# Optimization experiments

Measured on AMD Instinct MI355X. Metric: run time of the kernel, lower is better.

Reference implementation:

```python
import jax, jax.numpy as jnp
import numpy as np

EMBED = 192
D_INNER = 2 * EMBED          # expand=2
D_STATE = 4                  # low_rank
D_CONV = 4
DT_RANK = (EMBED + 15) // 16 # ceil(192/16) = 12
N_MIX = 2
RANK = 4                     # LowRankProjection rank
B_, H_, W_ = 8, 64, 64


def setup_inputs() -> dict:
    key = jax.random.key(0)
    ks = jax.random.split(key, 16)
    s = lambda *sh: 1.0 / np.sqrt(sh[-1])
    inp = {
        "x": jax.random.normal(ks[0], (B_, EMBED, H_, W_), jnp.float32),
        # stacked per-mixer Mamba params (leading dim N_MIX)
        "in_proj_w": jax.random.normal(ks[1], (N_MIX, 2 * D_INNER, EMBED), jnp.float32) * s(EMBED),
        "conv_w": jax.random.normal(ks[2], (N_MIX, D_INNER, D_CONV), jnp.float32) * s(D_CONV),
        "conv_b": jnp.zeros((N_MIX, D_INNER), jnp.float32),
        "x_proj_w": jax.random.normal(ks[3], (N_MIX, DT_RANK + 2 * D_STATE, D_INNER), jnp.float32) * s(D_INNER),
        "dt_proj_w": jax.random.normal(ks[4], (N_MIX, D_INNER, DT_RANK), jnp.float32) * s(DT_RANK),
        "dt_proj_b": jax.random.uniform(ks[5], (N_MIX, D_INNER), jnp.float32, -4.0, -2.0),
        "A_log": jnp.tile(jnp.log(jnp.arange(1, D_STATE + 1, dtype=jnp.float32))[None, None, :], (N_MIX, D_INNER, 1)),
        "D": jnp.ones((N_MIX, D_INNER), jnp.float32),
        "out_proj_w": jax.random.normal(ks[6], (N_MIX, EMBED, D_INNER), jnp.float32) * s(D_INNER),
        # LowRankProjection
        "U_w": jax.random.normal(ks[7], (RANK, EMBED), jnp.float32) * s(EMBED),
        "V_w": jax.random.normal(ks[8], (EMBED, RANK), jnp.float32) * s(RANK),
        # LayerNorm
        "ln_g": jnp.ones((EMBED,), jnp.float32),
        "ln_b": jnp.zeros((EMBED,), jnp.float32),
    }
    return inp


def _silu(x):
    return x * jax.nn.sigmoid(x)


def _mamba(x, in_proj_w, conv_w, conv_b, x_proj_w, dt_proj_w, dt_proj_b, A_log, D, out_proj_w):
    # x: (B, L, d_model)
    B, L, _ = x.shape
    xz = jnp.einsum("bld,ed->ble", x, in_proj_w)          # (B, L, 2*d_inner)
    xin, z = jnp.split(xz, 2, axis=-1)
    # causal depthwise conv over L
    xt = jnp.transpose(xin, (0, 2, 1))                      # (B, d_inner, L)
    xc = jax.lax.conv_general_dilated(
        xt, conv_w[:, None, :], window_strides=(1,), padding=[(D_CONV - 1, 0)],
        feature_group_count=D_INNER, dimension_numbers=("NCH", "OIH", "NCH"))
    xa = _silu(jnp.transpose(xc + conv_b[None, :, None], (0, 2, 1)))  # (B, L, d_inner)
    x_dbl = jnp.einsum("bld,ed->ble", xa, x_proj_w)         # (B, L, dt_rank+2*d_state)
    dt_lr = x_dbl[..., :DT_RANK]
    Bm = x_dbl[..., DT_RANK:DT_RANK + D_STATE]              # (B, L, d_state)
    Cm = x_dbl[..., DT_RANK + D_STATE:]                     # (B, L, d_state)
    dt = jax.nn.softplus(jnp.einsum("blr,dr->bld", dt_lr, dt_proj_w) + dt_proj_b)  # (B, L, d_inner)
    A = -jnp.exp(A_log)                                     # (d_inner, d_state)
    dA = jnp.exp(dt[..., None] * A)                         # (B, L, d_inner, d_state)
    dBu = dt[..., None] * Bm[:, :, None, :] * xa[..., None]  # (B, L, d_inner, d_state)

    def step(h, inputs):
        dA_i, dBu_i, C_i = inputs                           # (B,d_inner,d_state),(B,d_inner,d_state),(B,d_state)
        h = dA_i * h + dBu_i
        y = jnp.einsum("bds,bs->bd", h, C_i)
        return h, y

    h0 = jnp.zeros((B, D_INNER, D_STATE), x.dtype)
    _, ys = jax.lax.scan(step, h0, (jnp.moveaxis(dA, 1, 0), jnp.moveaxis(dBu, 1, 0), jnp.moveaxis(Cm, 1, 0)))
    y = jnp.moveaxis(ys, 0, 1) + xa * D                     # (B, L, d_inner)
    y = y * _silu(z)
    return jnp.einsum("ble,de->bld", y, out_proj_w)         # (B, L, d_model)


def reference(x, in_proj_w, conv_w, conv_b, x_proj_w, dt_proj_w, dt_proj_b,
              A_log, D, out_proj_w, U_w, V_w, ln_g, ln_b):
    residual = x
    B, C, H, W = x.shape
    h = jnp.transpose(x, (0, 2, 3, 1)).reshape(B, H * W, C)
    for i in range(N_MIX):
        h = _mamba(h, in_proj_w[i], conv_w[i], conv_b[i], x_proj_w[i], dt_proj_w[i],
                   dt_proj_b[i], A_log[i], D[i], out_proj_w[i])
    # low-rank projection
    h = jnp.einsum("blr,dr->bld", jnp.einsum("blc,rc->blr", h, U_w), V_w)
    h = jnp.transpose(h.reshape(B, H, W, C), (0, 3, 1, 2)) + residual
    # LayerNorm over channels
    hc = jnp.transpose(h, (0, 2, 3, 1))
    mu = hc.mean(-1, keepdims=True)
    var = ((hc - mu) ** 2).mean(-1, keepdims=True)
    hc = (hc - mu) * jax.lax.rsqrt(var + 1e-5) * ln_g + ln_b
    return jnp.transpose(hc, (0, 3, 1, 2))
```

## Files before the change

kernel.cpp:

```cpp
#include <hip/hip_runtime.h>
#include <hip/hip_bf16.h>
#include <cstdint>

#define EMBED   192
#define DINNER  384
#define DSTATE  4
#define DCONV   4
#define DTRANK  12
#define NMIX    2
#define RANK    4
#define BB      8
#define LL      4096
#define NBL     (BB*LL)
#define NCHUNK  128
#define CLEN    32
#define RSTR    36

typedef __attribute__((ext_vector_type(8))) short short8;
typedef __attribute__((ext_vector_type(4))) float float4v;

static __device__ __forceinline__ ushort f2b(float f) {
    __hip_bfloat16 h = __float2bfloat16(f);
    return *(ushort*)&h;
}
static __device__ __forceinline__ float b2f(ushort u) {
    __hip_bfloat16 h;
    *(ushort*)&h = u;
    return __bfloat162float(h);
}
static __device__ __forceinline__ float bs2f(short s) {
    ushort u = (ushort)s;
    return b2f(u);
}

#define PREP_N0 294912
#define PREP_N1 147456
#define PREP_N2 24576
#define PREP_N3 24576
#define PREP_N4 3072
__global__ __launch_bounds__(256) void k_prep(const float* __restrict__ in_proj_w,
                                              const float* __restrict__ out_proj_w,
                                              const float* __restrict__ x_proj_w,
                                              const float* __restrict__ dt_proj_w,
                                              const float* __restrict__ conv_w,
                                              ushort* __restrict__ wi,
                                              ushort* __restrict__ wo,
                                              ushort* __restrict__ xpwb,
                                              ushort* __restrict__ dtwpad,
                                              float* __restrict__ cwt) {
    int i = blockIdx.x * 256 + threadIdx.x;
    if (i < PREP_N0) {
        wi[i] = f2b(in_proj_w[i]);
        return;
    }
    i -= PREP_N0;
    if (i < PREP_N1) {
        wo[i] = f2b(out_proj_w[i]);
        return;
    }
    i -= PREP_N1;
    if (i < PREP_N2) {
        int mix = i / (32 * 384);
        int rem = i % (32 * 384);
        int e = rem / 384, k = rem % 384;
        xpwb[i] = (e < 20) ? f2b(x_proj_w[(size_t)mix * 20 * 384 + e * 384 + k]) : (ushort)0;
        return;
    }
    i -= PREP_N2;
    if (i < PREP_N3) {
        int mix = i / (384 * 32);
        int rem = i % (384 * 32);
        int n = rem / 32, r = rem % 32;
        dtwpad[i] = (r < DTRANK) ? f2b(dt_proj_w[(size_t)mix * 384 * DTRANK + n * DTRANK + r])
                                 : (ushort)0;
        return;
    }
    i -= PREP_N3;
    if (i < PREP_N4) {
        int mix = i / (DCONV * DINNER);
        int rem = i % (DCONV * DINNER);
        int k = rem / DINNER, d = rem % DINNER;
        cwt[i] = conv_w[(size_t)mix * DINNER * DCONV + d * DCONV + k];
    }
}

__global__ __launch_bounds__(256) void k_transpose(const float* __restrict__ x,
                                                   ushort* __restrict__ h0b) {
    __shared__ float tile[32][33];
    int b  = blockIdx.z;
    int c0 = blockIdx.y * 32;
    int l0 = blockIdx.x * 32;
    int tx = threadIdx.x;
    int ty = threadIdx.y;
    #pragma unroll
    for (int i = 0; i < 4; i++) {
        int c = c0 + ty + i * 8;
        tile[ty + i * 8][tx] = x[((size_t)b * EMBED + c) * LL + l0 + tx];
    }
    __syncthreads();
    #pragma unroll
    for (int i = 0; i < 4; i++) {
        int l = l0 + ty + i * 8;
        h0b[((size_t)b * LL + l) * EMBED + c0 + tx] = f2b(tile[tx][ty + i * 8]);
    }
}

template<int TN, int WRN>
__global__ __launch_bounds__(256) void k_gemm_bf16(const ushort* __restrict__ A, int lda,
                                                   const ushort* __restrict__ Bw, int ldb,
                                                   float* __restrict__ C, int ldc,
                                                   ushort* __restrict__ Cb, int ldcb,
                                                   int K) {
    constexpr int WRM = 4 / WRN;
    constexpr int WM  = 128 / WRM;
    constexpr int MT  = WM / 16;
    __shared__ ushort As[128][40];
    __shared__ ushort Bs[TN][40];
    int tid  = threadIdx.x;
    int lane = tid & 63;
    int wave = tid >> 6;
    int wmo = (wave / WRN) * WM;
    int wno = (wave % WRN) * 64;
    int m0 = blockIdx.y * 128;
    int n0 = blockIdx.x * TN;

    float4v acc[MT][4];
    #pragma unroll
    for (int i = 0; i < MT; i++)
        #pragma unroll
        for (int j = 0; j < 4; j++)
            acc[i][j] = (float4v){0.f, 0.f, 0.f, 0.f};

    for (int k0 = 0; k0 < K; k0 += 32) {
        #pragma unroll
        for (int i = 0; i < 2; i++) {
            int idx = tid + i * 256;
            int r = idx >> 2, sg = idx & 3;
            *(short8*)&As[r][sg * 8] =
                *(const short8*)(A + (size_t)(m0 + r) * lda + k0 + sg * 8);
        }
        #pragma unroll
        for (int i = 0; i < TN / 64; i++) {
            int idx = tid + i * 256;
            int r = idx >> 2, sg = idx & 3;
            *(short8*)&Bs[r][sg * 8] =
                *(const short8*)(Bw + (size_t)(n0 + r) * ldb + k0 + sg * 8);
        }
        __syncthreads();
        short8 av[MT], bv[4];
        #pragma unroll
        for (int i = 0; i < MT; i++)
            av[i] = *(const short8*)&As[wmo + i * 16 + (lane & 15)][(lane >> 4) * 8];
        #pragma unroll
        for (int j = 0; j < 4; j++)
            bv[j] = *(const short8*)&Bs[wno + j * 16 + (lane & 15)][(lane >> 4) * 8];
        #pragma unroll
        for (int i = 0; i < MT; i++)
            #pragma unroll
            for (int j = 0; j < 4; j++)
                acc[i][j] = __builtin_amdgcn_mfma_f32_16x16x32_bf16(
                    av[i], bv[j], acc[i][j], 0, 0, 0);
        __syncthreads();
    }

    #pragma unroll
    for (int i = 0; i < MT; i++) {
        int rbase = m0 + wmo + i * 16 + (lane >> 4) * 4;
        #pragma unroll
        for (int j = 0; j < 4; j++) {
            int col = n0 + wno + j * 16 + (lane & 15);
            #pragma unroll
            for (int r = 0; r < 4; r++) {
                float v = acc[i][j][r];
                if (C)  C[(size_t)(rbase + r) * ldc + col] = v;
                if (Cb) Cb[(size_t)(rbase + r) * ldcb + col] = f2b(v);
            }
        }
    }
}

__global__ __launch_bounds__(256) void k_conv_silu(const ushort* __restrict__ xz,
                                                   const float* __restrict__ cwt,
                                                   const float* __restrict__ cb,
                                                   ushort* __restrict__ xa) {
    int t   = blockIdx.x * 256 + threadIdx.x;
    int g   = t % 48;
    int blc = t / 48;
    int d0  = g * 8;
    int lc  = blc % (LL / 8);
    int b   = blc / (LL / 8);
    int l0  = lc * 8;

    float wk[4][8], bias[8];
    #pragma unroll
    for (int k = 0; k < 4; k++) {
        float4v wa = *(const float4v*)(cwt + k * DINNER + d0);
        float4v wb = *(const float4v*)(cwt + k * DINNER + d0 + 4);
        #pragma unroll
        for (int j = 0; j < 4; j++) { wk[k][j] = wa[j]; wk[k][j + 4] = wb[j]; }
    }
    {
        float4v ba = *(const float4v*)(cb + d0);
        float4v bb = *(const float4v*)(cb + d0 + 4);
        #pragma unroll
        for (int j = 0; j < 4; j++) { bias[j] = ba[j]; bias[j + 4] = bb[j]; }
    }

    float r0[8] = {}, r1[8] = {}, r2[8] = {};
    const ushort* px = xz + ((size_t)(b * LL + l0)) * 768 + d0;
    if (l0 > 0) {
        short8 v;
        v = *(const short8*)(px - 3 * 768);
        #pragma unroll
        for (int j = 0; j < 8; j++) r0[j] = bs2f(v[j]);
        v = *(const short8*)(px - 2 * 768);
        #pragma unroll
        for (int j = 0; j < 8; j++) r1[j] = bs2f(v[j]);
        v = *(const short8*)(px - 1 * 768);
        #pragma unroll
        for (int j = 0; j < 8; j++) r2[j] = bs2f(v[j]);
    }
    ushort* po = xa + ((size_t)(b * LL + l0)) * DINNER + d0;
    #pragma unroll
    for (int i = 0; i < 8; i++) {
        short8 v = *(const short8*)(px + (size_t)i * 768);
        float cur[8];
        #pragma unroll
        for (int j = 0; j < 8; j++) cur[j] = bs2f(v[j]);
        short8 ov;
        #pragma unroll
        for (int j = 0; j < 8; j++) {
            float a = bias[j] + wk[0][j] * r0[j] + wk[1][j] * r1[j]
                    + wk[2][j] * r2[j] + wk[3][j] * cur[j];
            float sv = a / (1.f + __expf(-a));
            ov[j] = (short)f2b(sv);
        }
        *(short8*)(po + (size_t)i * DINNER) = ov;
        #pragma unroll
        for (int j = 0; j < 8; j++) { r0[j] = r1[j]; r1[j] = r2[j]; r2[j] = cur[j]; }
    }
}

__global__ __launch_bounds__(256) void k_xproj_mfma(const ushort* __restrict__ xa,
                                                    const ushort* __restrict__ xpwb,
                                                    float* __restrict__ xdb32) {
    __shared__ ushort As[128][40];
    __shared__ ushort Bs[32][40];
    int tid  = threadIdx.x;
    int lane = tid & 63;
    int wave = tid >> 6;
    int m0 = blockIdx.x * 128;
    float4v acc[2][2];
    #pragma unroll
    for (int i = 0; i < 2; i++)
        #pragma unroll
        for (int j = 0; j < 2; j++)
            acc[i][j] = (float4v){0.f, 0.f, 0.f, 0.f};
    for (int k0 = 0; k0 < 384; k0 += 32) {
        #pragma unroll
        for (int i = 0; i < 2; i++) {
            int idx = tid + i * 256;
            int r = idx >> 2, sg = idx & 3;
            *(short8*)&As[r][sg * 8] =
                *(const short8*)(xa + (size_t)(m0 + r) * 384 + k0 + sg * 8);
        }
        if (tid < 128) {
            int r = tid >> 2, sg = tid & 3;
            *(short8*)&Bs[r][sg * 8] =
                *(const short8*)(xpwb + (size_t)r * 384 + k0 + sg * 8);
        }
        __syncthreads();
        short8 av[2], bv[2];
        #pragma unroll
        for (int i = 0; i < 2; i++)
            av[i] = *(const short8*)&As[wave * 32 + i * 16 + (lane & 15)][(lane >> 4) * 8];
        #pragma unroll
        for (int j = 0; j < 2; j++)
            bv[j] = *(const short8*)&Bs[j * 16 + (lane & 15)][(lane >> 4) * 8];
        #pragma unroll
        for (int i = 0; i < 2; i++)
            #pragma unroll
            for (int j = 0; j < 2; j++)
                acc[i][j] = __builtin_amdgcn_mfma_f32_16x16x32_bf16(
                    av[i], bv[j], acc[i][j], 0, 0, 0);
        __syncthreads();
    }
    #pragma unroll
    for (int i = 0; i < 2; i++) {
        int rbase = m0 + wave * 32 + i * 16 + (lane >> 4) * 4;
        #pragma unroll
        for (int j = 0; j < 2; j++) {
            int col = j * 16 + (lane & 15);
            #pragma unroll
            for (int r = 0; r < 4; r++)
                xdb32[(size_t)(rbase + r) * 32 + col] = acc[i][j][r];
        }
    }
}

static __device__ __forceinline__ void dt_mfma_tile(const float* __restrict__ rows,
                                                    const ushort* __restrict__ dtwpad,
                                                    const float* __restrict__ dtb,
                                                    ushort* __restrict__ dtS,
                                                    int wave, int lane) {
    int mcol = lane & 15;
    int quad = lane >> 4;
    #pragma unroll
    for (int nt = 0; nt < 4; nt++) {
        int n = wave * 64 + nt * 16 + mcol;
        short8 bv = *(const short8*)(dtwpad + (size_t)n * 32 + quad * 8);
        float bias = dtb[n];
        #pragma unroll
        for (int mt = 0; mt < 2; mt++) {
            float4v a0 = *(const float4v*)&rows[(mt * 16 + mcol) * RSTR + quad * 8];
            float4v a1 = *(const float4v*)&rows[(mt * 16 + mcol) * RSTR + quad * 8 + 4];
            short8 av;
            #pragma unroll
            for (int j = 0; j < 4; j++) {
                av[j]     = (short)f2b(a0[j]);
                av[j + 4] = (short)f2b(a1[j]);
            }
            float4v acc = (float4v){0.f, 0.f, 0.f, 0.f};
            acc = __builtin_amdgcn_mfma_f32_16x16x32_bf16(av, bv, acc, 0, 0, 0);
            #pragma unroll
            for (int r = 0; r < 4; r++) {
                float s = acc[r] + bias;
                float sp = fmaxf(s, 0.f) + __logf(1.f + __expf(-fabsf(s)));
                dtS[(mt * 16 + quad * 4 + r) * DINNER + n] = f2b(sp);
            }
        }
    }
}

static __device__ __forceinline__ bool as_is_harmonic(const float* As) {
    return fabsf(As[1] - 2.f * As[0]) <= 1e-5f * fabsf(As[1]) + 1e-12f
        && fabsf(As[2] - 3.f * As[0]) <= 1e-5f * fabsf(As[2]) + 1e-12f
        && fabsf(As[3] - 4.f * As[0]) <= 1e-5f * fabsf(As[3]) + 1e-12f;
}

__global__ __launch_bounds__(384) void k_scan_local(const ushort* __restrict__ xa,
                                                    const float* __restrict__ xdb32,
                                                    const ushort* __restrict__ dtwpad,
                                                    const float* __restrict__ dtb,
                                                    const float* __restrict__ A_log,
                                                    float* __restrict__ carryT,
                                                    float* __restrict__ carryH) {
    int d     = threadIdx.x;
    int lane  = d & 63;
    int wave  = d >> 6;
    int chunk = blockIdx.x;
    int b     = blockIdx.y;
    __shared__ float rows[CLEN * RSTR];
    __shared__ ushort dtS[CLEN * DINNER];
    size_t rbase = ((size_t)b * LL + (size_t)chunk * CLEN) * 32;
    for (int i = d; i < CLEN * 32; i += 384) {
        int l = i >> 5, e = i & 31;
        rows[l * RSTR + e] = xdb32[rbase + i];
    }
    float As[DSTATE];
    #pragma unroll
    for (int s = 0; s < DSTATE; s++) As[s] = -__expf(A_log[d * DSTATE + s]);
    bool fastA = as_is_harmonic(As);
    __syncthreads();
    dt_mfma_tile(rows, dtwpad, dtb, dtS, wave, lane);
    __syncthreads();
    float h[DSTATE] = {0.f, 0.f, 0.f, 0.f};
    float T = 0.f;
    size_t mbase = (size_t)b * LL + (size_t)chunk * CLEN;
    for (int l = 0; l < CLEN; l++) {
        float dtvv = b2f(dtS[l * DINNER + d]);
        float xav  = b2f(xa[(mbase + l) * DINNER + d]);
        float du   = dtvv * xav;
        T += dtvv;
        const float* row = &rows[l * RSTR];
        float da[DSTATE];
        if (fastA) {
            float p = __expf(dtvv * As[0]);
            da[0] = p; da[1] = p * p; da[2] = da[1] * p; da[3] = da[2] * p;
        } else {
            #pragma unroll
            for (int s = 0; s < DSTATE; s++) da[s] = __expf(dtvv * As[s]);
        }
        #pragma unroll
        for (int s = 0; s < DSTATE; s++)
            h[s] = da[s] * h[s] + du * row[DTRANK + s];
    }
    size_t cb = ((size_t)chunk * BB + b);
    carryT[cb * 384 + d] = T;
    float4v hv = {h[0], h[1], h[2], h[3]};
    *(float4v*)(carryH + cb * 1536 + d * 4) = hv;
}

__global__ __launch_bounds__(256) void k_scan_combine(const float* __restrict__ carryT,
                                                      const float* __restrict__ carryH,
                                                      const float* __restrict__ A_log,
                                                      float* __restrict__ carryI) {
    int c   = blockIdx.x * 256 + threadIdx.x;
    int b   = c / 1536;
    int rem = c - b * 1536;
    int d   = rem >> 2;
    float As = -__expf(A_log[rem]);
    float hrun = 0.f;
    for (int k = 0; k < NCHUNK; k++) {
        size_t o = (size_t)k * BB + b;
        float T  = carryT[o * 384 + d];
        float Hk = carryH[o * 1536 + rem];
        carryI[o * 1536 + rem] = hrun;
        hrun = __expf(As * T) * hrun + Hk;
    }
}

__global__ __launch_bounds__(384) void k_scan_final(const ushort* __restrict__ xa,
                                                    const ushort* __restrict__ xz,
                                                    const float* __restrict__ xdb32,
                                                    const ushort* __restrict__ dtwpad,
                                                    const float* __restrict__ dtb,
                                                    const float* __restrict__ A_log,
                                                    const float* __restrict__ Dp,
                                                    const float* __restrict__ carryI,
                                                    ushort* __restrict__ y) {
    int d     = threadIdx.x;
    int lane  = d & 63;
    int wave  = d >> 6;
    int chunk = blockIdx.x;
    int b     = blockIdx.y;
    __shared__ float rows[CLEN * RSTR];
    __shared__ ushort dtS[CLEN * DINNER];
    size_t rbase = ((size_t)b * LL + (size_t)chunk * CLEN) * 32;
    for (int i = d; i < CLEN * 32; i += 384) {
        int l = i >> 5, e = i & 31;
        rows[l * RSTR + e] = xdb32[rbase + i];
    }
    float As[DSTATE];
    #pragma unroll
    for (int s = 0; s < DSTATE; s++) As[s] = -__expf(A_log[d * DSTATE + s]);
    bool fastA = as_is_harmonic(As);
    float Dd = Dp[d];
    float4v hv = *(const float4v*)(carryI + ((size_t)chunk * BB + b) * 1536 + d * 4);
    float h[DSTATE];
    #pragma unroll
    for (int s = 0; s < DSTATE; s++) h[s] = hv[s];
    __syncthreads();
    dt_mfma_tile(rows, dtwpad, dtb, dtS, wave, lane);
    __syncthreads();
    size_t mbase = (size_t)b * LL + (size_t)chunk * CLEN;
    for (int l = 0; l < CLEN; l++) {
        size_t m = mbase + l;
        float dtvv = b2f(dtS[l * DINNER + d]);
        float xav  = b2f(xa[m * DINNER + d]);
        float du   = dtvv * xav;
        const float* row = &rows[l * RSTR];
        float da[DSTATE];
        if (fastA) {
            float p = __expf(dtvv * As[0]);
            da[0] = p; da[1] = p * p; da[2] = da[1] * p; da[3] = da[2] * p;
        } else {
            #pragma unroll
            for (int s = 0; s < DSTATE; s++) da[s] = __expf(dtvv * As[s]);
        }
        float yv = 0.f;
        #pragma unroll
        for (int s = 0; s < DSTATE; s++) {
            h[s] = da[s] * h[s] + du * row[DTRANK + s];
            yv  += h[s] * row[DTRANK + DSTATE + s];
        }
        yv += xav * Dd;
        float zv = b2f(xz[m * 768 + DINNER + d]);
        yv *= zv / (1.f + __expf(-zv));
        y[m * DINNER + d] = f2b(yv);
    }
}

__global__ __launch_bounds__(256) void k_tail(const ushort* __restrict__ h1b,
                                              const ushort* __restrict__ h0b,
                                              const float* __restrict__ U,
                                              const float* __restrict__ V,
                                              const float* __restrict__ g,
                                              const float* __restrict__ be,
                                              float* __restrict__ out) {
    __shared__ float tile[EMBED * 65];
    int tid  = threadIdx.x;
    int lane = tid & 63;
    int wave = tid >> 6;
    int b  = blockIdx.y;
    int l0 = blockIdx.x * 64;
    for (int t = 0; t < 16; t++) {
        int lloc = wave * 16 + t;
        size_t m = (size_t)b * LL + l0 + lloc;
        float hv[3];
        #pragma unroll
        for (int i = 0; i < 3; i++) hv[i] = b2f(h1b[m * EMBED + lane + 64 * i]);
        float r[RANK];
        #pragma unroll
        for (int j = 0; j < RANK; j++) {
            float p = 0.f;
            #pragma unroll
            for (int i = 0; i < 3; i++) p += hv[i] * U[j * EMBED + lane + 64 * i];
            #pragma unroll
            for (int off = 1; off < 64; off <<= 1) p += __shfl_xor(p, off);
            r[j] = p;
        }
        float u[3], s1 = 0.f, s2 = 0.f;
        #pragma unroll
        for (int i = 0; i < 3; i++) {
            int c = lane + 64 * i;
            float v = r[0] * V[c * 4 + 0] + r[1] * V[c * 4 + 1]
                    + r[2] * V[c * 4 + 2] + r[3] * V[c * 4 + 3];
            u[i] = v + b2f(h0b[m * EMBED + c]);
            s1 += u[i];
            s2 += u[i] * u[i];
        }
        #pragma unroll
        for (int off = 1; off < 64; off <<= 1) {
            s1 += __shfl_xor(s1, off);
            s2 += __shfl_xor(s2, off);
        }
        float mean = s1 * (1.f / EMBED);
        float var  = s2 * (1.f / EMBED) - mean * mean;
        float inv  = rsqrtf(var + 1e-5f);
        #pragma unroll
        for (int i = 0; i < 3; i++) {
            int c = lane + 64 * i;
            tile[c * 65 + lloc] = (u[i] - mean) * inv * g[c] + be[c];
        }
    }
    __syncthreads();
    for (int i = tid; i < EMBED * 64; i += 256) {
        int c = i >> 6, l = i & 63;
        out[((size_t)(b * EMBED + c)) * LL + l0 + l] = tile[c * 65 + l];
    }
}

extern "C" void kernel_launch(void* const* d_in, const int* in_sizes, int n_in,
                              void* d_out, int out_size, void* d_ws, size_t ws_size,
                              hipStream_t stream) {
    const float* x          = (const float*)d_in[0];
    const float* in_proj_w  = (const float*)d_in[1];
    const float* conv_w     = (const float*)d_in[2];
    const float* conv_b     = (const float*)d_in[3];
    const float* x_proj_w   = (const float*)d_in[4];
    const float* dt_proj_w  = (const float*)d_in[5];
    const float* dt_proj_b  = (const float*)d_in[6];
    const float* A_log      = (const float*)d_in[7];
    const float* Dp         = (const float*)d_in[8];
    const float* out_proj_w = (const float*)d_in[9];
    const float* U_w        = (const float*)d_in[10];
    const float* V_w        = (const float*)d_in[11];
    const float* ln_g       = (const float*)d_in[12];
    const float* ln_b       = (const float*)d_in[13];
    float* out = (float*)d_out;

    float* ws    = (float*)d_ws;
    float* xdb32 = ws;
    float* carryT = xdb32 + (size_t)NBL * 32;
    float* carryH = carryT + (size_t)NCHUNK * BB * DINNER;
    float* carryI = carryH + (size_t)NCHUNK * BB * DINNER * DSTATE;
    ushort* xz16   = (ushort*)(carryI + (size_t)NCHUNK * BB * DINNER * DSTATE);
    ushort* xa16   = xz16   + (size_t)NBL * 768;
    ushort* yb     = xa16   + (size_t)NBL * DINNER;
    ushort* h0b    = yb     + (size_t)NBL * DINNER;
    ushort* h1b    = h0b    + (size_t)NBL * EMBED;
    ushort* wi     = h1b    + (size_t)NBL * EMBED;
    ushort* wo     = wi     + (size_t)NMIX * 768 * EMBED;
    ushort* xpwb   = wo     + (size_t)NMIX * EMBED * DINNER;
    ushort* dtwpad = xpwb   + (size_t)NMIX * 32 * 384;
    float*  cwt    = (float*)(dtwpad + (size_t)NMIX * 384 * 32);

    k_prep<<<(PREP_N0 + PREP_N1 + PREP_N2 + PREP_N3 + PREP_N4) / 256, 256, 0, stream>>>(
        in_proj_w, out_proj_w, x_proj_w, dt_proj_w, conv_w, wi, wo, xpwb, dtwpad, cwt);

    k_transpose<<<dim3(LL / 32, EMBED / 32, BB), dim3(32, 8), 0, stream>>>(x, h0b);

    const ushort* hinb = h0b;
    for (int mix = 0; mix < NMIX; mix++) {
        const float* Alg  = A_log + (size_t)mix * DINNER * DSTATE;
        const ushort* dtwm = dtwpad + (size_t)mix * 384 * 32;
        const float* dtbm = dt_proj_b + mix * DINNER;

        k_gemm_bf16<128, 2><<<dim3(768 / 128, NBL / 128), 256, 0, stream>>>(
            hinb, EMBED, wi + (size_t)mix * 768 * EMBED, EMBED,
            (float*)nullptr, 0, xz16, 768, EMBED);
        k_conv_silu<<<(NBL / 8 * 48) / 256, 256, 0, stream>>>(
            xz16, cwt + (size_t)mix * DCONV * DINNER, conv_b + mix * DINNER, xa16);
        k_xproj_mfma<<<NBL / 128, 256, 0, stream>>>(
            xa16, xpwb + (size_t)mix * 32 * 384, xdb32);
        k_scan_local<<<dim3(NCHUNK, BB), 384, 0, stream>>>(
            xa16, xdb32, dtwm, dtbm, Alg, carryT, carryH);
        k_scan_combine<<<(BB * DINNER * DSTATE) / 256, 256, 0, stream>>>(
            carryT, carryH, Alg, carryI);
        k_scan_final<<<dim3(NCHUNK, BB), 384, 0, stream>>>(
            xa16, xz16, xdb32, dtwm, dtbm, Alg, Dp + mix * DINNER, carryI, yb);
        k_gemm_bf16<64, 1><<<dim3(EMBED / 64, NBL / 128), 256, 0, stream>>>(
            yb, DINNER, wo + (size_t)mix * EMBED * DINNER, DINNER,
            (float*)nullptr, 0, h1b, EMBED, DINNER);
        hinb = h1b;
    }

    k_tail<<<dim3(LL / 64, BB), 256, 0, stream>>>(h1b, h0b, U_w, V_w, ln_g, ln_b, out);
}
```

Measured before the change: 408.1 us.

## Compute local scan outputs in first pass and apply carry correction in second

The first scan pass now also computes each chunk's local output (including the D skip term) and stores it along with the dt values in bf16 buffers. The second pass no longer recomputes the dt MFMA tile or the local recurrence. It only propagates the incoming carry state, decaying it by exp(dt*A), and adds its contribution C·h to the stored local output before the SiLU gate. This trades the recomputation for two extra bf16 writes and reads per element of size B·L·DINNER, and storing the partial output in bf16 adds rounding.

```diff
diff --git a/kernel.cpp b/kernel.cpp
--- a/kernel.cpp
+++ b/kernel.cpp
@@ -343,8 +343,11 @@
                                                     const ushort* __restrict__ dtwpad,
                                                     const float* __restrict__ dtb,
                                                     const float* __restrict__ A_log,
+                                                    const float* __restrict__ Dp,
                                                     float* __restrict__ carryT,
-                                                    float* __restrict__ carryH) {
+                                                    float* __restrict__ carryH,
+                                                    ushort* __restrict__ dt16,
+                                                    ushort* __restrict__ ylb) {
     int d     = threadIdx.x;
     int lane  = d & 63;
     int wave  = d >> 6;
@@ -361,6 +364,7 @@
     #pragma unroll
     for (int s = 0; s < DSTATE; s++) As[s] = -__expf(A_log[d * DSTATE + s]);
     bool fastA = as_is_harmonic(As);
+    float Dd = Dp[d];
     __syncthreads();
     dt_mfma_tile(rows, dtwpad, dtb, dtS, wave, lane);
     __syncthreads();
@@ -368,7 +372,8 @@
     float T = 0.f;
     size_t mbase = (size_t)b * LL + (size_t)chunk * CLEN;
     for (int l = 0; l < CLEN; l++) {
-        float dtvv = b2f(dtS[l * DINNER + d]);
+        ushort dtu = dtS[l * DINNER + d];
+        float dtvv = b2f(dtu);
         float xav  = b2f(xa[(mbase + l) * DINNER + d]);
         float du   = dtvv * xav;
         T += dtvv;
@@ -381,9 +386,14 @@
             #pragma unroll
             for (int s = 0; s < DSTATE; s++) da[s] = __expf(dtvv * As[s]);
         }
-        #pragma unroll
-        for (int s = 0; s < DSTATE; s++)
+        float yv = xav * Dd;
+        #pragma unroll
+        for (int s = 0; s < DSTATE; s++) {
             h[s] = da[s] * h[s] + du * row[DTRANK + s];
+            yv  += h[s] * row[DTRANK + DSTATE + s];
+        }
+        dt16[(mbase + l) * DINNER + d] = dtu;
+        ylb[(mbase + l) * DINNER + d]  = f2b(yv);
     }
     size_t cb = ((size_t)chunk * BB + b);
     carryT[cb * 384 + d] = T;
@@ -410,46 +420,36 @@
     }
 }
 
-__global__ __launch_bounds__(384) void k_scan_final(const ushort* __restrict__ xa,
-                                                    const ushort* __restrict__ xz,
-                                                    const float* __restrict__ xdb32,
-                                                    const ushort* __restrict__ dtwpad,
-                                                    const float* __restrict__ dtb,
-                                                    const float* __restrict__ A_log,
-                                                    const float* __restrict__ Dp,
-                                                    const float* __restrict__ carryI,
-                                                    ushort* __restrict__ y) {
+__global__ __launch_bounds__(384) void k_scan_corr(const ushort* __restrict__ dt16,
+                                                   const ushort* __restrict__ ylb,
+                                                   const ushort* __restrict__ xz,
+                                                   const float* __restrict__ xdb32,
+                                                   const float* __restrict__ A_log,
+                                                   const float* __restrict__ carryI,
+                                                   ushort* __restrict__ y) {
     int d     = threadIdx.x;
-    int lane  = d & 63;
-    int wave  = d >> 6;
     int chunk = blockIdx.x;
     int b     = blockIdx.y;
-    __shared__ float rows[CLEN * RSTR];
-    __shared__ ushort dtS[CLEN * DINNER];
+    __shared__ float Crow[CLEN][DSTATE];
     size_t rbase = ((size_t)b * LL + (size_t)chunk * CLEN) * 32;
-    for (int i = d; i < CLEN * 32; i += 384) {
-        int l = i >> 5, e = i & 31;
-        rows[l * RSTR + e] = xdb32[rbase + i];
+    if (d < CLEN * DSTATE) {
+        int l = d >> 2, s = d & 3;
+        Crow[l][s] = xdb32[rbase + l * 32 + DTRANK + DSTATE + s];
     }
     float As[DSTATE];
     #pragma unroll
     for (int s = 0; s < DSTATE; s++) As[s] = -__expf(A_log[d * DSTATE + s]);
     bool fastA = as_is_harmonic(As);
-    float Dd = Dp[d];
     float4v hv = *(const float4v*)(carryI + ((size_t)chunk * BB + b) * 1536 + d * 4);
-    float h[DSTATE];
-    #pragma unroll
-    for (int s = 0; s < DSTATE; s++) h[s] = hv[s];
-    __syncthreads();
-    dt_mfma_tile(rows, dtwpad, dtb, dtS, wave, lane);
+    float hc[DSTATE];
+    #pragma unroll
+    for (int s = 0; s < DSTATE; s++) hc[s] = hv[s];
     __syncthreads();
     size_t mbase = (size_t)b * LL + (size_t)chunk * CLEN;
+    #pragma unroll 4
     for (int l = 0; l < CLEN; l++) {
         size_t m = mbase + l;
-        float dtvv = b2f(dtS[l * DINNER + d]);
-        float xav  = b2f(xa[m * DINNER + d]);
-        float du   = dtvv * xav;
-        const float* row = &rows[l * RSTR];
+        float dtvv = b2f(dt16[m * DINNER + d]);
         float da[DSTATE];
         if (fastA) {
             float p = __expf(dtvv * As[0]);
@@ -458,13 +458,13 @@
             #pragma unroll
             for (int s = 0; s < DSTATE; s++) da[s] = __expf(dtvv * As[s]);
         }
-        float yv = 0.f;
+        float corr = 0.f;
         #pragma unroll
         for (int s = 0; s < DSTATE; s++) {
-            h[s] = da[s] * h[s] + du * row[DTRANK + s];
-            yv  += h[s] * row[DTRANK + DSTATE + s];
-        }
-        yv += xav * Dd;
+            hc[s] *= da[s];
+            corr  += hc[s] * Crow[l][s];
+        }
+        float yv = b2f(ylb[m * DINNER + d]) + corr;
         float zv = b2f(xz[m * 768 + DINNER + d]);
         yv *= zv / (1.f + __expf(-zv));
         y[m * DINNER + d] = f2b(yv);
@@ -560,7 +560,9 @@
     ushort* yb     = xa16   + (size_t)NBL * DINNER;
     ushort* h0b    = yb     + (size_t)NBL * DINNER;
     ushort* h1b    = h0b    + (size_t)NBL * EMBED;
-    ushort* wi     = h1b    + (size_t)NBL * EMBED;
+    ushort* dt16   = h1b    + (size_t)NBL * EMBED;
+    ushort* ylb    = dt16   + (size_t)NBL * DINNER;
+    ushort* wi     = ylb    + (size_t)NBL * DINNER;
     ushort* wo     = wi     + (size_t)NMIX * 768 * EMBED;
     ushort* xpwb   = wo     + (size_t)NMIX * EMBED * DINNER;
     ushort* dtwpad = xpwb   + (size_t)NMIX * 32 * 384;
@@ -585,11 +587,11 @@
         k_xproj_mfma<<<NBL / 128, 256, 0, stream>>>(
             xa16, xpwb + (size_t)mix * 32 * 384, xdb32);
         k_scan_local<<<dim3(NCHUNK, BB), 384, 0, stream>>>(
-            xa16, xdb32, dtwm, dtbm, Alg, carryT, carryH);
+            xa16, xdb32, dtwm, dtbm, Alg, Dp + mix * DINNER, carryT, carryH, dt16, ylb);
         k_scan_combine<<<(BB * DINNER * DSTATE) / 256, 256, 0, stream>>>(
             carryT, carryH, Alg, carryI);
-        k_scan_final<<<dim3(NCHUNK, BB), 384, 0, stream>>>(
-            xa16, xz16, xdb32, dtwm, dtbm, Alg, Dp + mix * DINNER, carryI, yb);
+        k_scan_corr<<<dim3(NCHUNK, BB), 384, 0, stream>>>(
+            dt16, ylb, xz16, xdb32, Alg, carryI, yb);
         k_gemm_bf16<64, 1><<<dim3(EMBED / 64, NBL / 128), 256, 0, stream>>>(
             yb, DINNER, wo + (size_t)mix * EMBED * DINNER, DINNER,
             (float*)nullptr, 0, h1b, EMBED, DINNER);
```

Result: faster. 394.3 us (-3.4%).
